# Kernel optimization log

Hardware: AMD Instinct MI355X
Metric: run time of the kernel (lower is better)

The kernel has to match this reference:

```python
import jax, jax.numpy as jnp
import numpy as np
import math

ATTN_C = 32
HEADS = 8
IN_C = 256
PAIR_C = 128
B, M, N = 1, 128, 256


def _layernorm(x, w, b, eps=1e-5):
    mu = jnp.mean(x, axis=-1, keepdims=True)
    xc = x - mu
    var = jnp.mean(xc * xc, axis=-1, keepdims=True)
    return xc * jax.lax.rsqrt(var + eps) * w + b


def setup_inputs() -> dict:
    key = jax.random.key(0)
    ks = jax.random.split(key, 10)
    s1 = 1.0 / math.sqrt(IN_C)
    s2 = 1.0 / math.sqrt(PAIR_C)
    s3 = 1.0 / math.sqrt(ATTN_C * HEADS)
    return {
        "x1d": jax.random.normal(ks[0], (B, M, N, IN_C), jnp.float32),
        "x2d": jax.random.normal(ks[1], (B, N, N, PAIR_C), jnp.float32),
        "norm_w": jnp.ones((IN_C,), jnp.float32),
        "norm_b": jnp.zeros((IN_C,), jnp.float32),
        "qkv_w": jax.random.normal(ks[2], (3 * ATTN_C * HEADS, IN_C), jnp.float32) * s1,
        "x2d_w": jax.random.normal(ks[3], (HEADS, PAIR_C), jnp.float32) * s2,
        "gate_w": jax.random.normal(ks[4], (ATTN_C * HEADS, IN_C), jnp.float32) * s1,
        "gate_b": jnp.zeros((ATTN_C * HEADS,), jnp.float32),
        "final_w": jax.random.normal(ks[5], (IN_C, ATTN_C * HEADS), jnp.float32) * s3,
        "final_b": jnp.zeros((IN_C,), jnp.float32),
    }


def reference(x1d, x2d, norm_w, norm_b, qkv_w, x2d_w, gate_w, gate_b, final_w, final_b):
    c, h = ATTN_C, HEADS
    x = _layernorm(x1d, norm_w, norm_b)                      # [B,M,N,IN_C]
    qkv = (x @ qkv_w.T).reshape(*x.shape[:-1], c, 3 * h)     # [B,M,N,c,3h]
    q, k, v = qkv[..., :h], qkv[..., h:2 * h], qkv[..., 2 * h:]
    aff = jnp.einsum('bmich,bmjch->bmijh', q, k)             # [B,M,N,N,H]
    gate = jax.nn.sigmoid(x @ gate_w.T + gate_b).reshape(*x.shape[:-1], c, h)
    factor = 1.0 / math.sqrt(c)
    bias = (x2d @ x2d_w.T) * factor                          # [B,N,N,H]
    weights = jax.nn.softmax(aff + bias[:, None], axis=-2)   # softmax over j
    out = jnp.einsum('bmrch,bmirh->bmich', v, weights) * gate
    out = out.reshape(*x.shape[:-1], c * h) @ final_w.T + final_b
    return out
```

## Files before the change

kernel.cpp:

```cpp
#include <hip/hip_runtime.h>
#include <math.h>

typedef short bf16x8 __attribute__((ext_vector_type(8)));
typedef float f32x4  __attribute__((ext_vector_type(4)));

#define NPOS 32768

#define OFF_CHI   0u
#define OFF_AHI   100663296u
#define OFF_ATTN  134217728u
#define OFF_BIAST 150994944u
#define OFF_WHI   153354240u
#define OFF_W2P   154402816u
#define OFF_GBP   154533888u

__device__ __forceinline__ short f2bf(float x) {
    unsigned int u = __float_as_uint(x);
    unsigned int r = (u + 0x7FFFu + ((u >> 16) & 1u)) >> 16;
    return (short)r;
}
__device__ __forceinline__ float bf2f(short s) {
    return __uint_as_float(((unsigned int)(unsigned short)s) << 16);
}
__device__ __forceinline__ void async_copy16(const void* g, void* l) {
    __builtin_amdgcn_global_load_lds(
        (const __attribute__((address_space(1))) unsigned int*)g,
        (__attribute__((address_space(3))) unsigned int*)l, 16, 0, 0);
}

__global__ void k_ln_cast(const float* __restrict__ x,
                          const float* __restrict__ nw, const float* __restrict__ nb,
                          short* __restrict__ Ahi) {
    int wid = (blockIdx.x * blockDim.x + threadIdx.x) >> 6;
    int lane = threadIdx.x & 63;
    const float4 v = ((const float4*)(x + (size_t)wid * 256))[lane];
    float s  = v.x + v.y + v.z + v.w;
    float ss = v.x*v.x + v.y*v.y + v.z*v.z + v.w*v.w;
    #pragma unroll
    for (int o = 32; o; o >>= 1) {
        s  += __shfl_xor(s,  o, 64);
        ss += __shfl_xor(ss, o, 64);
    }
    float mu  = s * (1.0f / 256);
    float var = ss * (1.0f / 256) - mu * mu;
    float rs  = rsqrtf(var + 1e-5f);
    const float4 wv = ((const float4*)nw)[lane];
    const float4 bv = ((const float4*)nb)[lane];
    float y[4] = {(v.x - mu) * rs * wv.x + bv.x, (v.y - mu) * rs * wv.y + bv.y,
                  (v.z - mu) * rs * wv.z + bv.z, (v.w - mu) * rs * wv.w + bv.w};
    short h4[4];
    #pragma unroll
    for (int i = 0; i < 4; ++i) h4[i] = f2bf(y[i]);
    *(short4*)(Ahi + (size_t)wid * 256 + lane * 4) = *(short4*)h4;
}

__global__ void k_castw(const float* __restrict__ qkvw, const float* __restrict__ gatew,
                        const float* __restrict__ gateb, const float* __restrict__ finalw,
                        short* __restrict__ Whi, short* __restrict__ W2p,
                        float* __restrict__ gbp) {
    int r = blockIdx.x, t = threadIdx.x;
    if (r < 1024) {
        int which = r >> 8, h = (r >> 5) & 7, c = r & 31;
        const float* src = (which < 3) ? qkvw + (size_t)(c * 24 + which * 8 + h) * 256
                                       : gatew + (size_t)(c * 8 + h) * 256;
        Whi[(size_t)r * 256 + t] = f2bf(src[t]);
    } else if (r < 1280) {
        int o = r - 1024;
        int h = t >> 5, c = t & 31;
        W2p[(size_t)o * 256 + t] = f2bf(finalw[(size_t)o * 256 + c * 8 + h]);
    } else {
        int h = t >> 5, c = t & 31;
        gbp[t] = gateb[c * 8 + h];
    }
}

__global__ __launch_bounds__(256) void k_bias2(const float* __restrict__ x2d,
                                               const float* __restrict__ x2dw,
                                               float* __restrict__ biasT) {
    __shared__ float xs[64][132];
    __shared__ float ws[8][132];
    const int t = threadIdx.x;
    const int wid0 = blockIdx.x * 64;
    #pragma unroll
    for (int r = 0; r < 8; ++r) {
        int g = r * 256 + t;
        int row = g >> 5, c4 = g & 31;
        float4 v = *(const float4*)(x2d + (size_t)(wid0 + row) * 128 + c4 * 4);
        *(float4*)&xs[row][c4 * 4] = v;
    }
    {
        int h = t >> 5, c4 = t & 31;
        *(float4*)&ws[h][c4 * 4] = *(const float4*)(x2dw + h * 128 + c4 * 4);
    }
    __syncthreads();
    const float f = 0.17677669529663687f;
    const int i = wid0 >> 8;
    #pragma unroll
    for (int kk = 0; kk < 2; ++kk) {
        int o = t + kk * 256;
        int row = o >> 3, h = o & 7;
        float acc = 0.f;
        #pragma unroll
        for (int c4 = 0; c4 < 32; ++c4) {
            float4 xv = *(const float4*)&xs[row][c4 * 4];
            float4 wv = *(const float4*)&ws[h][c4 * 4];
            acc += xv.x * wv.x + xv.y * wv.y + xv.z * wv.z + xv.w * wv.w;
        }
        int j = (wid0 & 255) + row;
        biasT[(((h * 256 + j)) << 8) + i] = acc * f;
    }
}

__global__ __launch_bounds__(256) void k_gemm1m(
    const short* __restrict__ Ahi, const short* __restrict__ Whi,
    const float* __restrict__ gbp, short* __restrict__ Chi) {
    __shared__ short As[128 * 64];
    __shared__ short Bs[128 * 64];
    const int t = threadIdx.x;
    const int wave = t >> 6, lane = t & 63, ln15 = lane & 15, quad = lane >> 4;
    const int posBase = blockIdx.x * 128;
    const int nb = blockIdx.y;
    const int i0w = (wave & 1) * 64, n0w = (wave >> 1) * 64;

    f32x4 acc[4][4];
    #pragma unroll
    for (int a = 0; a < 4; ++a)
        #pragma unroll
        for (int b = 0; b < 4; ++b) acc[a][b] = (f32x4){0.f, 0.f, 0.f, 0.f};

    for (int k0 = 0; k0 < 256; k0 += 64) {
        #pragma unroll
        for (int r = 0; r < 4; ++r) {
            int g = r * 256 + t;
            int row = g >> 3, cs = g & 7;
            int colg = cs ^ (row & 7);
            size_t aoff = (size_t)(posBase + row) * 256 + k0 + colg * 8;
            size_t boff = (size_t)(nb * 128 + row) * 256 + k0 + colg * 8;
            int ldst = (r * 256 + wave * 64) * 8;
            async_copy16(Ahi + aoff, &As[ldst]);
            async_copy16(Whi + boff, &Bs[ldst]);
        }
        __syncthreads();
        #pragma unroll
        for (int kc = 0; kc < 2; ++kc) {
            bf16x8 af[4], bfr[4];
            #pragma unroll
            for (int it = 0; it < 4; ++it) {
                int rowa = i0w + it * 16 + ln15;
                int c8a = (kc * 4 + quad) ^ (rowa & 7);
                af[it] = *(const bf16x8*)&As[rowa * 64 + c8a * 8];
                int rowb = n0w + it * 16 + ln15;
                int c8b = (kc * 4 + quad) ^ (rowb & 7);
                bfr[it] = *(const bf16x8*)&Bs[rowb * 64 + c8b * 8];
            }
            #pragma unroll
            for (int it = 0; it < 4; ++it)
                #pragma unroll
                for (int nt = 0; nt < 4; ++nt)
                    acc[it][nt] = __builtin_amdgcn_mfma_f32_16x16x32_bf16(
                        bfr[nt], af[it], acc[it][nt], 0, 0, 0);
        }
        __syncthreads();
    }
    const bool isgate = (nb >= 6);
    #pragma unroll
    for (int it = 0; it < 4; ++it) {
        size_t pos = posBase + i0w + it * 16 + ln15;
        #pragma unroll
        for (int nt = 0; nt < 4; ++nt) {
            int ncol0 = nb * 128 + n0w + nt * 16 + quad * 4;
            float v[4];
            #pragma unroll
            for (int r = 0; r < 4; ++r) v[r] = acc[it][nt][r];
            if (isgate) {
                const float4 gb = *(const float4*)&gbp[ncol0 - 768];
                v[0] = 1.0f / (1.0f + __expf(-(v[0] + gb.x)));
                v[1] = 1.0f / (1.0f + __expf(-(v[1] + gb.y)));
                v[2] = 1.0f / (1.0f + __expf(-(v[2] + gb.z)));
                v[3] = 1.0f / (1.0f + __expf(-(v[3] + gb.w)));
            }
            unsigned w0 = (unsigned)(unsigned short)f2bf(v[0])
                        | ((unsigned)(unsigned short)f2bf(v[1]) << 16);
            unsigned w1 = (unsigned)(unsigned short)f2bf(v[2])
                        | ((unsigned)(unsigned short)f2bf(v[3]) << 16);
            *(uint2*)&Chi[pos * 1024 + ncol0] = make_uint2(w0, w1);
        }
    }
}

__global__ __launch_bounds__(512) void k_attn3(
    const short* __restrict__ Chi, const float* __restrict__ biasT,
    short* __restrict__ attnB) {
    __shared__ short Khi[256 * 32];
    __shared__ short VT[32 * 264];

    const int mh = blockIdx.x;
    const int m = mh >> 3, h = mh & 7;
    const int t = threadIdx.x;
    const int wave = t >> 6, lane = t & 63, ln15 = lane & 15, quad = lane >> 4;
    const int i0 = wave * 32;

    #pragma unroll
    for (int r = 0; r < 2; ++r) {
        int g = r * 512 + t;
        int j = g >> 2, c16 = g & 3;
        int cs = c16 ^ (j & 3);
        const short* gp = Chi + (size_t)(m * 256 + j) * 1024 + 256 + h * 32 + cs * 8;
        async_copy16(gp, &Khi[(r * 512 + wave * 64) * 8]);
    }
    {
        int j = t & 255, c0 = (t >> 8) * 16;
        const short* vp = Chi + (size_t)(m * 256 + j) * 1024 + 512 + h * 32 + c0;
        bf16x8 v0 = *(const bf16x8*)vp;
        bf16x8 v1 = *(const bf16x8*)(vp + 8);
        #pragma unroll
        for (int c = 0; c < 8; ++c) VT[(c0 + c) * 264 + j] = v0[c];
        #pragma unroll
        for (int c = 0; c < 8; ++c) VT[(c0 + 8 + c) * 264 + j] = v1[c];
    }
    bf16x8 qhi[2];
    #pragma unroll
    for (int it = 0; it < 2; ++it) {
        int i = i0 + it * 16 + ln15;
        qhi[it] = *(const bf16x8*)(Chi + (size_t)(m * 256 + i) * 1024 + h * 32 + quad * 8);
    }
    __syncthreads();

    const int srcA = ln15 + ((quad & 1) << 5);
    const int srcB = srcA + 16;
    const bool lowj = (quad < 2);

    float lacc[2] = {0.f, 0.f};
    f32x4 Oacc[2][2];
    #pragma unroll
    for (int a = 0; a < 2; ++a) {
        Oacc[a][0] = (f32x4){0.f, 0.f, 0.f, 0.f};
        Oacc[a][1] = (f32x4){0.f, 0.f, 0.f, 0.f};
    }
    const float* bp = biasT + (size_t)h * 65536;

    for (int j0 = 0; j0 < 256; j0 += 32) {
        bf16x8 kfh[2], vf[2];
        #pragma unroll
        for (int jt = 0; jt < 2; ++jt) {
            int j = j0 + jt * 16 + ln15;
            int cs = quad ^ (j & 3);
            kfh[jt] = *(const bf16x8*)&Khi[j * 32 + cs * 8];
        }
        #pragma unroll
        for (int ct = 0; ct < 2; ++ct) {
            int c = ct * 16 + ln15;
            vf[ct] = *(const bf16x8*)&VT[c * 264 + j0 + quad * 8];
        }
        #pragma unroll
        for (int it = 0; it < 2; ++it) {
            int i = i0 + it * 16 + ln15;
            float b0[4], b1[4];
            #pragma unroll
            for (int r = 0; r < 4; ++r) {
                b0[r] = bp[(j0 + quad * 4 + r) * 256 + i];
                b1[r] = bp[(j0 + 16 + quad * 4 + r) * 256 + i];
            }
            f32x4 s0 = (f32x4){0.f, 0.f, 0.f, 0.f};
            f32x4 s1 = (f32x4){0.f, 0.f, 0.f, 0.f};
            s0 = __builtin_amdgcn_mfma_f32_16x16x32_bf16(kfh[0], qhi[it], s0, 0, 0, 0);
            s1 = __builtin_amdgcn_mfma_f32_16x16x32_bf16(kfh[1], qhi[it], s1, 0, 0, 0);
            float p[8], ps = 0.f;
            #pragma unroll
            for (int r = 0; r < 4; ++r) { p[r] = __expf(s0[r] + b0[r]); ps += p[r]; }
            #pragma unroll
            for (int r = 0; r < 4; ++r) { p[4 + r] = __expf(s1[r] + b1[r]); ps += p[4 + r]; }
            lacc[it] += ps;
            unsigned w0 = (unsigned)(unsigned short)f2bf(p[0])
                        | ((unsigned)(unsigned short)f2bf(p[1]) << 16);
            unsigned w1 = (unsigned)(unsigned short)f2bf(p[2])
                        | ((unsigned)(unsigned short)f2bf(p[3]) << 16);
            unsigned w2 = (unsigned)(unsigned short)f2bf(p[4])
                        | ((unsigned)(unsigned short)f2bf(p[5]) << 16);
            unsigned w3 = (unsigned)(unsigned short)f2bf(p[6])
                        | ((unsigned)(unsigned short)f2bf(p[7]) << 16);
            unsigned a0 = __shfl(w0, srcA, 64), a1 = __shfl(w1, srcA, 64);
            unsigned a2 = __shfl(w2, srcA, 64), a3 = __shfl(w3, srcA, 64);
            unsigned c0 = __shfl(w0, srcB, 64), c1 = __shfl(w1, srcB, 64);
            unsigned c2 = __shfl(w2, srcB, 64), c3 = __shfl(w3, srcB, 64);
            unsigned pd[4];
            pd[0] = lowj ? a0 : a2;
            pd[1] = lowj ? a1 : a3;
            pd[2] = lowj ? c0 : c2;
            pd[3] = lowj ? c1 : c3;
            bf16x8 pf = *(const bf16x8*)pd;
            Oacc[it][0] = __builtin_amdgcn_mfma_f32_16x16x32_bf16(pf, vf[0], Oacc[it][0], 0, 0, 0);
            Oacc[it][1] = __builtin_amdgcn_mfma_f32_16x16x32_bf16(pf, vf[1], Oacc[it][1], 0, 0, 0);
        }
    }
    #pragma unroll
    for (int it = 0; it < 2; ++it) {
        float l = lacc[it];
        l += __shfl_xor(l, 16, 64);
        l += __shfl_xor(l, 32, 64);
        float inv = 1.0f / l;
        float invr[4];
        #pragma unroll
        for (int r = 0; r < 4; ++r) invr[r] = __shfl(inv, quad * 4 + r, 16);
        #pragma unroll
        for (int ct = 0; ct < 2; ++ct) {
            int c = ct * 16 + ln15;
            #pragma unroll
            for (int r = 0; r < 4; ++r) {
                int i = i0 + it * 16 + quad * 4 + r;
                float g = bf2f(Chi[(size_t)(m * 256 + i) * 1024 + 768 + h * 32 + c]);
                float val = Oacc[it][ct][r] * invr[r] * g;
                attnB[(size_t)(m * 256 + i) * 256 + h * 32 + c] = f2bf(val);
            }
        }
    }
}

__global__ __launch_bounds__(256) void k_gemm2m(
    const short* __restrict__ A, const short* __restrict__ W2p,
    const float* __restrict__ fb, float* __restrict__ out) {
    __shared__ short As[128 * 64];
    __shared__ short Bs[128 * 64];
    const int t = threadIdx.x;
    const int wave = t >> 6, lane = t & 63, ln15 = lane & 15, quad = lane >> 4;
    const int posBase = blockIdx.x * 128;
    const int nb = blockIdx.y;
    const int i0w = (wave & 1) * 64, n0w = (wave >> 1) * 64;

    f32x4 acc[4][4];
    #pragma unroll
    for (int a = 0; a < 4; ++a)
        #pragma unroll
        for (int b = 0; b < 4; ++b) acc[a][b] = (f32x4){0.f, 0.f, 0.f, 0.f};

    for (int k0 = 0; k0 < 256; k0 += 64) {
        #pragma unroll
        for (int r = 0; r < 4; ++r) {
            int g = r * 256 + t;
            int row = g >> 3, cs = g & 7;
            int colg = cs ^ (row & 7);
            const short* ga = A + (size_t)(posBase + row) * 256 + k0 + colg * 8;
            async_copy16(ga, &As[(r * 256 + wave * 64) * 8]);
            const short* gb = W2p + (size_t)(nb * 128 + row) * 256 + k0 + colg * 8;
            async_copy16(gb, &Bs[(r * 256 + wave * 64) * 8]);
        }
        __syncthreads();
        #pragma unroll
        for (int kc = 0; kc < 2; ++kc) {
            bf16x8 af[4], bfr[4];
            #pragma unroll
            for (int it = 0; it < 4; ++it) {
                int rowa = i0w + it * 16 + ln15;
                int c8a = (kc * 4 + quad) ^ (rowa & 7);
                af[it] = *(const bf16x8*)&As[rowa * 64 + c8a * 8];
                int rowb = n0w + it * 16 + ln15;
                int c8b = (kc * 4 + quad) ^ (rowb & 7);
                bfr[it] = *(const bf16x8*)&Bs[rowb * 64 + c8b * 8];
            }
            #pragma unroll
            for (int it = 0; it < 4; ++it)
                #pragma unroll
                for (int nt = 0; nt < 4; ++nt)
                    acc[it][nt] = __builtin_amdgcn_mfma_f32_16x16x32_bf16(
                        bfr[nt], af[it], acc[it][nt], 0, 0, 0);
        }
        __syncthreads();
    }
    #pragma unroll
    for (int it = 0; it < 4; ++it) {
        size_t pos = posBase + i0w + it * 16 + ln15;
        #pragma unroll
        for (int nt = 0; nt < 4; ++nt) {
            int ncol0 = nb * 128 + n0w + nt * 16 + quad * 4;
            const float4 fbv = *(const float4*)&fb[ncol0];
            float4 o;
            o.x = acc[it][nt][0] + fbv.x;
            o.y = acc[it][nt][1] + fbv.y;
            o.z = acc[it][nt][2] + fbv.z;
            o.w = acc[it][nt][3] + fbv.w;
            *(float4*)&out[pos * 256 + ncol0] = o;
        }
    }
}

extern "C" void kernel_launch(void* const* d_in, const int* in_sizes, int n_in,
                              void* d_out, int out_size, void* d_ws, size_t ws_size,
                              hipStream_t stream) {
    const float* x1d     = (const float*)d_in[0];
    const float* x2d     = (const float*)d_in[1];
    const float* norm_w  = (const float*)d_in[2];
    const float* norm_b  = (const float*)d_in[3];
    const float* qkv_w   = (const float*)d_in[4];
    const float* x2d_w   = (const float*)d_in[5];
    const float* gate_w  = (const float*)d_in[6];
    const float* gate_b  = (const float*)d_in[7];
    const float* final_w = (const float*)d_in[8];
    const float* final_b = (const float*)d_in[9];
    float* out = (float*)d_out;
    char* w = (char*)d_ws;

    short* Chi   = (short*)(w + OFF_CHI);
    short* Ahi   = (short*)(w + OFF_AHI);
    short* attnB = (short*)(w + OFF_ATTN);
    float* biasT = (float*)(w + OFF_BIAST);
    short* Whi   = (short*)(w + OFF_WHI);
    short* W2p   = (short*)(w + OFF_W2P);
    float* gbp   = (float*)(w + OFF_GBP);

    k_ln_cast<<<NPOS / 4, 256, 0, stream>>>(x1d, norm_w, norm_b, Ahi);
    k_castw<<<1281, 256, 0, stream>>>(qkv_w, gate_w, gate_b, final_w, Whi, W2p, gbp);
    k_bias2<<<1024, 256, 0, stream>>>(x2d, x2d_w, biasT);
    k_gemm1m<<<dim3(256, 8), 256, 0, stream>>>(Ahi, Whi, gbp, Chi);
    k_attn3<<<1024, 512, 0, stream>>>(Chi, biasT, attnB);
    k_gemm2m<<<dim3(256, 2), 256, 0, stream>>>(attnB, W2p, final_b, out);
}
```

Before: 227.2 us.

## Double-buffer LDS tiles in projection GEMM to overlap async loads with MFMA

The QKV/gate projection GEMM now uses two LDS buffers per operand. It issues the async global-to-LDS copy for the next K slice before computing the current one, with explicit vmcnt waits and raw s_barriers in place of __syncthreads. This is meant to hide global load latency behind the MFMA work. It doubles the kernel's LDS use, which may lower occupancy, and it relies on the vmcnt count matching the eight copies each thread issues per stage.

Result: faster. 222.4 us (-2.1%).

```diff
diff --git a/kernel.cpp b/kernel.cpp
--- a/kernel.cpp
+++ b/kernel.cpp
@@ -114,8 +114,8 @@
 __global__ __launch_bounds__(256) void k_gemm1m(
     const short* __restrict__ Ahi, const short* __restrict__ Whi,
     const float* __restrict__ gbp, short* __restrict__ Chi) {
-    __shared__ short As[128 * 64];
-    __shared__ short Bs[128 * 64];
+    __shared__ short As[2][128 * 64];
+    __shared__ short Bs[2][128 * 64];
     const int t = threadIdx.x;
     const int wave = t >> 6, lane = t & 63, ln15 = lane & 15, quad = lane >> 4;
     const int posBase = blockIdx.x * 128;
@@ -128,7 +128,7 @@
         #pragma unroll
         for (int b = 0; b < 4; ++b) acc[a][b] = (f32x4){0.f, 0.f, 0.f, 0.f};
 
-    for (int k0 = 0; k0 < 256; k0 += 64) {
+    auto stage = [&](int buf, int k0) {
         #pragma unroll
         for (int r = 0; r < 4; ++r) {
             int g = r * 256 + t;
@@ -137,10 +137,24 @@
             size_t aoff = (size_t)(posBase + row) * 256 + k0 + colg * 8;
             size_t boff = (size_t)(nb * 128 + row) * 256 + k0 + colg * 8;
             int ldst = (r * 256 + wave * 64) * 8;
-            async_copy16(Ahi + aoff, &As[ldst]);
-            async_copy16(Whi + boff, &Bs[ldst]);
-        }
-        __syncthreads();
+            async_copy16(Ahi + aoff, &As[buf][ldst]);
+            async_copy16(Whi + boff, &Bs[buf][ldst]);
+        }
+    };
+
+    stage(0, 0);
+    #pragma unroll
+    for (int ks = 0; ks < 4; ++ks) {
+        const int cur = ks & 1;
+        if (ks < 3) {
+            stage(cur ^ 1, (ks + 1) * 64);
+            asm volatile("s_waitcnt vmcnt(8)" ::: "memory");
+        } else {
+            asm volatile("s_waitcnt vmcnt(0)" ::: "memory");
+        }
+        __builtin_amdgcn_sched_barrier(0);
+        __builtin_amdgcn_s_barrier();
+        __builtin_amdgcn_sched_barrier(0);
         #pragma unroll
         for (int kc = 0; kc < 2; ++kc) {
             bf16x8 af[4], bfr[4];
@@ -148,10 +162,10 @@
             for (int it = 0; it < 4; ++it) {
                 int rowa = i0w + it * 16 + ln15;
                 int c8a = (kc * 4 + quad) ^ (rowa & 7);
-                af[it] = *(const bf16x8*)&As[rowa * 64 + c8a * 8];
+                af[it] = *(const bf16x8*)&As[cur][rowa * 64 + c8a * 8];
                 int rowb = n0w + it * 16 + ln15;
                 int c8b = (kc * 4 + quad) ^ (rowb & 7);
-                bfr[it] = *(const bf16x8*)&Bs[rowb * 64 + c8b * 8];
+                bfr[it] = *(const bf16x8*)&Bs[cur][rowb * 64 + c8b * 8];
             }
             #pragma unroll
             for (int it = 0; it < 4; ++it)
@@ -160,7 +174,9 @@
                     acc[it][nt] = __builtin_amdgcn_mfma_f32_16x16x32_bf16(
                         bfr[nt], af[it], acc[it][nt], 0, 0, 0);
         }
-        __syncthreads();
+        __builtin_amdgcn_sched_barrier(0);
+        __builtin_amdgcn_s_barrier();
+        __builtin_amdgcn_sched_barrier(0);
     }
     const bool isgate = (nb >= 6);
     #pragma unroll
```
